# Kernel optimization log

Measured on AMD Instinct MI355X. Metric: run time of the kernel, lower is better.

The kernel has to match this reference:

```python
import jax, jax.numpy as jnp
import numpy as np

NA, NV, FEAT = 8000, 4000, 32
H, D = 4, 16            # heads, per-head dim
HD = H * D              # 64 node width
BLOCKS, DEPTH = 6, 2    # 12 attention layers total
OUT = 64
AK, AVK, VK = 10, 15, 15
EPS = 1e-5


def setup_inputs() -> dict:
    key = jax.random.key(0)
    ks = jax.random.split(key, 16)
    rn = lambda k, s, sc=0.1: (jax.random.normal(k, s, dtype=jnp.float32) * sc)
    return {
        "atom_x": rn(ks[0], (NA, FEAT), 1.0),
        "atom_pos": rn(ks[1], (NA, 3), 1.0),
        "vox_x": rn(ks[2], (NV, FEAT), 1.0),
        "vox_pos": rn(ks[3], (NV, 3), 1.0),
        "W_atom_in": rn(ks[4], (FEAT, HD)),
        "b_atom_in": jnp.zeros((HD,), jnp.float32),
        "W_vox_in": rn(ks[5], (FEAT, HD)),
        "b_vox_in": jnp.zeros((HD,), jnp.float32),
        "emlp_w1": rn(ks[6], (3, 1, 8), 0.5),
        "emlp_b1": jnp.zeros((3, 8), jnp.float32),
        "emlp_w2": rn(ks[7], (3, 8, 1), 0.5),
        "emlp_b2": jnp.zeros((3, 1), jnp.float32),
        "ln_g": jnp.ones((BLOCKS * DEPTH, HD), jnp.float32),
        "ln_b": jnp.zeros((BLOCKS * DEPTH, HD), jnp.float32),
        "Ws": rn(ks[8], (BLOCKS * DEPTH, HD, HD)),
        "Wd": rn(ks[9], (BLOCKS * DEPTH, HD, HD)),
        "We": rn(ks[10], (BLOCKS * DEPTH, 1, HD)),
        "att": rn(ks[11], (BLOCKS * DEPTH, H, D)),
        "Wo1": rn(ks[12], ((BLOCKS + 1) * HD, HD)),
        "bo1": jnp.zeros((HD,), jnp.float32),
        "Wo2": rn(ks[13], (HD, OUT)),
        "bo2": jnp.zeros((OUT,), jnp.float32),
    }


def _knn_edges(q_pos, c_pos, k, q_off, c_off):
    # for each query, k nearest candidates (single-graph batch)
    d2 = (jnp.sum(q_pos * q_pos, 1, keepdims=True)
          - 2.0 * q_pos @ c_pos.T
          + jnp.sum(c_pos * c_pos, 1))                      # [Nq, Nc]
    idx = jax.lax.top_k(-d2, k)[1]                          # [Nq, k]
    src = (idx + c_off).reshape(-1)
    dst = jnp.repeat(jnp.arange(q_pos.shape[0]) + q_off, k)
    return src, dst


def _forward(atom_x, atom_pos, vox_x, vox_pos,
             W_atom_in, b_atom_in, W_vox_in, b_vox_in,
             emlp_w1, emlp_b1, emlp_w2, emlp_b2,
             ln_g, ln_b, Ws, Wd, We, att, Wo1, bo1, Wo2, bo2):
    Na, Nv = atom_x.shape[0], vox_x.shape[0]
    N = Na + Nv
    x = jnp.concatenate([atom_x @ W_atom_in + b_atom_in,
                         vox_x @ W_vox_in + b_vox_in], 0)   # [N, HD]
    pos = jnp.concatenate([atom_pos, vox_pos], 0)           # [N, 3]

    # (query_pos, cand_pos, k, q_offset, c_offset, edge-MLP index)
    combos = [(atom_pos, atom_pos, AK, 0, 0, 0),    # atom<-atom
              (atom_pos, vox_pos, AVK, 0, Na, 1),   # atom<-vox
              (vox_pos, vox_pos, VK, Na, Na, 2)]    # vox<-vox
    srcs, dsts, attrs = [], [], []
    for qp, cp, k, qo, co, mi in combos:
        s, d = _knn_edges(qp, cp, k, qo, co)
        dist = jnp.linalg.norm(pos[s] - pos[d], axis=1, keepdims=True)  # [E,1]
        h = jax.nn.relu(dist @ emlp_w1[mi] + emlp_b1[mi])
        attrs.append(h @ emlp_w2[mi] + emlp_b2[mi])
        srcs.append(s); dsts.append(d)
    src = jnp.concatenate(srcs)
    dst = jnp.concatenate(dsts)
    eattr = jnp.concatenate(attrs, 0)                       # [E,1]

    def gat_layer(xin, l):
        mu = xin.mean(-1, keepdims=True)
        var = xin.var(-1, keepdims=True)
        h = (xin - mu) * jax.lax.rsqrt(var + EPS) * ln_g[l] + ln_b[l]
        s = (h @ Ws[l]).reshape(N, H, D)
        d_ = (h @ Wd[l]).reshape(N, H, D)
        e = (eattr @ We[l]).reshape(-1, H, D)
        m = s[src] + d_[dst] + e                            # [E,H,D]
        score = jnp.einsum('ehd,hd->eh', jax.nn.leaky_relu(m, 0.2), att[l])
        smax = jax.ops.segment_max(score, dst, num_segments=N)
        a = jnp.exp(score - smax[dst])
        denom = jax.ops.segment_sum(a, dst, num_segments=N)
        alpha = a / denom[dst]                              # softmax per dst node
        msg = jax.ops.segment_sum(alpha[..., None] * s[src], dst,
                                  num_segments=N).reshape(N, HD)
        return jax.nn.relu(xin + msg)

    outs = [x]
    cur = x
    for b in range(BLOCKS):
        for dd in range(DEPTH):
            cur = gat_layer(cur, b * DEPTH + dd)
        outs.append(cur)
    cat = jnp.concatenate(outs, -1)[Na:]                    # vox nodes, [Nv,448]
    enc = jax.nn.relu(cat @ Wo1 + bo1) @ Wo2 + bo2          # [Nv,OUT]
    return enc


def reference(atom_x, atom_pos, vox_x, vox_pos,
              W_atom_in, b_atom_in, W_vox_in, b_vox_in,
              emlp_w1, emlp_b1, emlp_w2, emlp_b2,
              ln_g, ln_b, Ws, Wd, We, att, Wo1, bo1, Wo2, bo2):
    enc = _forward(atom_x, atom_pos, vox_x, vox_pos,
                   W_atom_in, b_atom_in, W_vox_in, b_vox_in,
                   emlp_w1, emlp_b1, emlp_w2, emlp_b2,
                   ln_g, ln_b, Ws, Wd, We, att, Wo1, bo1, Wo2, bo2)
    return (enc, vox_pos)
```

## Files before the change

kernel.cpp:

```cpp
#include <hip/hip_runtime.h>
#include <math.h>

#define NA 8000
#define NV 4000
#define NN 12000
#define NA_PAD 8192
#define NV_PAD 4096
#define KNN_TILE 2048
#define FEAT 32
#define HD 64
#define NLAYER 12
#define E_AA 80000
#define E_AV 120000
#define E_VV 60000
#define E_TOT 260000
#define ENC_SIZE (NV * HD)
#define EPS 1e-5f
#define NGRP (NN/4)

__device__ __forceinline__ float wave_sum64(float v) {
#pragma unroll
  for (int off = 1; off < 64; off <<= 1) v += __shfl_xor(v, off);
  return v;
}

__device__ __forceinline__ float dpp_step(float v, const int ctrl) {
  int p;
  switch (ctrl) {
    case 0xB1:  p = __builtin_amdgcn_update_dpp(0, __float_as_int(v), 0xB1,  0xF, 0xF, true); break;
    case 0x4E:  p = __builtin_amdgcn_update_dpp(0, __float_as_int(v), 0x4E,  0xF, 0xF, true); break;
    case 0x141: p = __builtin_amdgcn_update_dpp(0, __float_as_int(v), 0x141, 0xF, 0xF, true); break;
    default:    p = __builtin_amdgcn_update_dpp(0, __float_as_int(v), 0x140, 0xF, 0xF, true); break;
  }
  return v + __int_as_float(p);
}

__device__ __forceinline__ float head_sum16_dpp(float v) {
  v = dpp_step(v, 0xB1);
  v = dpp_step(v, 0x4E);
  v = dpp_step(v, 0x141);
  v = dpp_step(v, 0x140);
  return v;
}

__device__ __forceinline__ float wave_sum64_dpp(float v) {
  v = head_sum16_dpp(v);
  v += __shfl_xor(v, 16);
  v += __shfl_xor(v, 32);
  return v;
}

__device__ __forceinline__ float dpp_shr1_f(float v) {
  const int p = __builtin_amdgcn_update_dpp(0, __float_as_int(v), 0x138, 0xF, 0xF, true);
  return __int_as_float(p);
}
__device__ __forceinline__ int dpp_shr1_i(int v) {
  return __builtin_amdgcn_update_dpp(0, v, 0x138, 0xF, 0xF, true);
}

__global__ __launch_bounds__(256) void pack_kernel(
    const float* __restrict__ apos, const float* __restrict__ vpos,
    float4* __restrict__ apk, float4* __restrict__ vpk)
{
  const int i = blockIdx.x * 256 + threadIdx.x;
  if (i < NA_PAD) {
    float4 r;
    if (i < NA) {
      const float cx = apos[i*3+0], cy = apos[i*3+1], cz = apos[i*3+2];
      r = make_float4(cx, cy, cz, (cx*cx + cy*cy) + cz*cz);
    } else r = make_float4(0.f, 0.f, 0.f, INFINITY);
    apk[i] = r;
  } else {
    const int j = i - NA_PAD;
    if (j < NV_PAD) {
      float4 r;
      if (j < NV) {
        const float cx = vpos[j*3+0], cy = vpos[j*3+1], cz = vpos[j*3+2];
        r = make_float4(cx, cy, cz, (cx*cx + cy*cy) + cz*cz);
      } else r = make_float4(0.f, 0.f, 0.f, INFINITY);
      vpk[j] = r;
    }
  }
}

#define KNN_INS(D2, JB)                                                \
  {                                                                    \
    unsigned long long m = __ballot((D2) < thrD);                      \
    if (m) {                                                           \
      do {                                                             \
        const int sl = __ffsll(m) - 1;                                 \
        m &= (m - 1ULL);                                               \
        const float v  = __shfl((D2), sl);                             \
        const int   vi = (JB) + sl;                                    \
        const bool stay = (eD < v) || (eD == v && eI < vi);            \
        const float pD = dpp_shr1_f(eD);                               \
        const int   pI = dpp_shr1_i(eI);                               \
        int pS = dpp_shr1_i(stay ? 1 : 0);                             \
        if (lane == 0) pS = 1;                                         \
        eD = stay ? eD : (pS ? v  : pD);                               \
        eI = stay ? eI : (pS ? vi : pI);                               \
      } while (m);                                                     \
      thrD = __shfl(eD, K-1);                                          \
    }                                                                  \
  }

template<int K, int NC_PAD>
__device__ __attribute__((noinline)) void knn_body(
    const float* __restrict__ qpos, const float4* __restrict__ cpk,
    int c_off, int* __restrict__ out_src, int qblock)
{
  extern __shared__ float4 tile[];
  const int tid  = threadIdx.x;
  const int wid  = tid >> 6, lane = tid & 63;
  const int q    = qblock * 8 + wid;
  const float qx = qpos[q*3+0], qy = qpos[q*3+1], qz = qpos[q*3+2];
  float qt = __fmul_rn(qx, qx);
  qt = __fmaf_rn(qy, qy, qt);
  const float qq = __fmaf_rn(qz, qz, qt);

  float eD = INFINITY; int eI = 0x7fffffff;
  float thrD = INFINITY;

  for (int t0 = 0; t0 < NC_PAD; t0 += KNN_TILE) {
    __syncthreads();
#pragma unroll
    for (int s = 0; s < KNN_TILE/512; ++s)
      tile[s*512 + tid] = cpk[t0 + s*512 + tid];
    __syncthreads();
#pragma unroll
    for (int it = 0; it < KNN_TILE/256; ++it) {
      const int b = it*256;
      const float4 c0 = tile[b +   0 + lane];
      const float4 c1 = tile[b +  64 + lane];
      const float4 c2 = tile[b + 128 + lane];
      const float4 c3 = tile[b + 192 + lane];
      float u0 = __fmul_rn(qx, c0.x); u0 = __fmaf_rn(qy, c0.y, u0);
      const float dot0 = __fmaf_rn(qz, c0.z, u0);
      const float d20  = __fadd_rn(__fmaf_rn(-2.0f, dot0, qq), c0.w);
      float u1 = __fmul_rn(qx, c1.x); u1 = __fmaf_rn(qy, c1.y, u1);
      const float dot1 = __fmaf_rn(qz, c1.z, u1);
      const float d21  = __fadd_rn(__fmaf_rn(-2.0f, dot1, qq), c1.w);
      float u2 = __fmul_rn(qx, c2.x); u2 = __fmaf_rn(qy, c2.y, u2);
      const float dot2 = __fmaf_rn(qz, c2.z, u2);
      const float d22  = __fadd_rn(__fmaf_rn(-2.0f, dot2, qq), c2.w);
      float u3 = __fmul_rn(qx, c3.x); u3 = __fmaf_rn(qy, c3.y, u3);
      const float dot3 = __fmaf_rn(qz, c3.z, u3);
      const float d23  = __fadd_rn(__fmaf_rn(-2.0f, dot3, qq), c3.w);
      const float dmin = fminf(fminf(d20, d21), fminf(d22, d23));
      if (__ballot(dmin < thrD)) {
        KNN_INS(d20, t0 + b +   0)
        KNN_INS(d21, t0 + b +  64)
        KNN_INS(d22, t0 + b + 128)
        KNN_INS(d23, t0 + b + 192)
      }
    }
  }
  if (lane < K) out_src[q*K + lane] = eI + c_off;
}

__global__ __launch_bounds__(512) void knn_all_kernel(
    const float* __restrict__ apos, const float* __restrict__ vpos,
    const float4* __restrict__ apk, const float4* __restrict__ vpk,
    int* __restrict__ srcA, int* __restrict__ srcAV, int* __restrict__ srcVV)
{
  const int b = blockIdx.x;
  if (b < NA/8)
    knn_body<10, NA_PAD>(apos, apk, 0,  srcA,  b);
  else if (b < 2*(NA/8))
    knn_body<15, NV_PAD>(apos, vpk, NA, srcAV, b - NA/8);
  else
    knn_body<15, NV_PAD>(vpos, vpk, NA, srcVV, b - 2*(NA/8));
}

__device__ __forceinline__ void ln_sd(
    float v, int node, int lane, int l,
    const float* __restrict__ ln_g, const float* __restrict__ ln_b,
    const float* __restrict__ Ws, const float* __restrict__ Wd,
    float* __restrict__ sbuf, float* __restrict__ dbuf)
{
  const float m = wave_sum64_dpp(v) * (1.0f/64.0f);
  const float c = v - m;
  const float var = wave_sum64_dpp(c*c) * (1.0f/64.0f);
  const float hn = c * rsqrtf(var + EPS) * ln_g[l*HD + lane] + ln_b[l*HD + lane];
  const float* ws = Ws + (size_t)l*HD*HD;
  const float* wd = Wd + (size_t)l*HD*HD;
  float accs = 0.0f, accd = 0.0f;
#pragma unroll
  for (int j = 0; j < HD; ++j) {
    const float hj = __shfl(hn, j);
    accs += hj * ws[j*HD + lane];
    accd += hj * wd[j*HD + lane];
  }
  sbuf[node*HD + lane] = accs;
  dbuf[node*HD + lane] = accd;
}

__global__ __launch_bounds__(64) void init_kernel(
    const float* __restrict__ atom_x, const float* __restrict__ vox_x,
    const float* __restrict__ Wa, const float* __restrict__ ba,
    const float* __restrict__ Wv, const float* __restrict__ bv,
    const float* __restrict__ ln_g, const float* __restrict__ ln_b,
    const float* __restrict__ Ws, const float* __restrict__ Wd,
    float* __restrict__ x, float* __restrict__ snap0,
    float* __restrict__ sbuf, float* __restrict__ dbuf)
{
  const int node = blockIdx.x;
  const int t    = threadIdx.x;
  const float* in; const float* W; const float* b;
  if (node < NA) { in = atom_x + node*FEAT;     W = Wa; b = ba; }
  else           { in = vox_x + (node-NA)*FEAT; W = Wv; b = bv; }
  float acc = b[t];
#pragma unroll
  for (int j = 0; j < FEAT; ++j) acc += in[j] * W[j*HD + t];
  x[node*HD + t] = acc;
  if (node >= NA) snap0[(node-NA)*HD + t] = acc;
  ln_sd(acc, node, t, 0, ln_g, ln_b, Ws, Wd, sbuf, dbuf);
}

__device__ __forceinline__ void load_pos(const float* ap, const float* vp,
                                         int i, float& px, float& py, float& pz)
{
  const float* p = (i < NA) ? (ap + i*3) : (vp + (i - NA)*3);
  px = p[0]; py = p[1]; pz = p[2];
}

__global__ __launch_bounds__(256) void edge_attr_kernel(
    const float* __restrict__ atom_pos, const float* __restrict__ vox_pos,
    const int* __restrict__ srcA, const int* __restrict__ srcAV,
    const int* __restrict__ srcVV,
    const float* __restrict__ w1, const float* __restrict__ b1,
    const float* __restrict__ w2, const float* __restrict__ b2,
    float* __restrict__ eattr)
{
  const int e = blockIdx.x * 256 + threadIdx.x;
  if (e >= E_TOT) return;
  int s, d, mi;
  if (e < E_AA)              { mi = 0; s = srcA[e];                 d = e / 10; }
  else if (e < E_AA + E_AV)  { mi = 1; const int t = e - E_AA;      s = srcAV[t]; d = t / 15; }
  else                       { mi = 2; const int t = e - E_AA - E_AV; s = srcVV[t]; d = NA + t / 15; }
  float sx, sy, sz, dx_, dy_, dz_;
  load_pos(atom_pos, vox_pos, s, sx, sy, sz);
  load_pos(atom_pos, vox_pos, d, dx_, dy_, dz_);
  const float ex = sx - dx_, ey = sy - dy_, ez = sz - dz_;
  const float dist = sqrtf(ex*ex + ey*ey + ez*ez);
  float acc = b2[mi];
#pragma unroll
  for (int j = 0; j < 8; ++j) {
    float h = dist * w1[mi*8 + j] + b1[mi*8 + j];
    h = (h > 0.0f) ? h : 0.0f;
    acc += h * w2[mi*8 + j];
  }
  eattr[e] = acc;
}

template<int NE, bool IS_ATOM>
__device__ __forceinline__ float agg_node(
    int n, int lane,
    float* __restrict__ x,
    const float* __restrict__ sbuf, const float* __restrict__ dbuf,
    const float* __restrict__ eattr,
    const int* __restrict__ srcA, const int* __restrict__ srcAV,
    const int* __restrict__ srcVV,
    const float* __restrict__ We, const float* __restrict__ att, int l,
    float* __restrict__ snap)
{
  const float wet  = We[l*HD + lane];
  const float attv = att[l*HD + lane];
  const float dn   = dbuf[n*HD + lane];

  int esrc[NE]; float eat[NE];
#pragma unroll
  for (int e = 0; e < NE; ++e) {
    int src, eidx;
    if (IS_ATOM) {
      if (e < 10) { src = srcA[n*10 + e];       eidx = n*10 + e; }
      else        { src = srcAV[n*15 + (e-10)]; eidx = E_AA + n*15 + (e-10); }
    } else {
      const int nv = n - NA;
      src = srcVV[nv*15 + e]; eidx = E_AA + E_AV + nv*15 + e;
    }
    esrc[e] = src;
    eat[e]  = eattr[eidx];
  }

  float srow[NE];
#pragma unroll
  for (int e = 0; e < NE; ++e) srow[e] = sbuf[esrc[e]*HD + lane];

  float escore[NE];
#pragma unroll
  for (int e = 0; e < NE; ++e) {
    float mm = srow[e] + dn + eat[e] * wet;
    mm = (mm >= 0.0f) ? mm : 0.2f * mm;
    escore[e] = head_sum16_dpp(mm * attv);
  }
  float mx = -INFINITY;
#pragma unroll
  for (int e = 0; e < NE; ++e) mx = fmaxf(mx, escore[e]);
  float den = 0.0f;
#pragma unroll
  for (int e = 0; e < NE; ++e) {
    const float a = __expf(escore[e] - mx);
    escore[e] = a; den += a;
  }
  const float inv = 1.0f / den;
  float msg = 0.0f;
#pragma unroll
  for (int e = 0; e < NE; ++e) msg += (escore[e] * inv) * srow[e];
  float xv = x[n*HD + lane] + msg;
  xv = (xv > 0.0f) ? xv : 0.0f;
  x[n*HD + lane] = xv;
  if (!IS_ATOM && snap != nullptr) snap[(n - NA)*HD + lane] = xv;
  return xv;
}

__global__ __launch_bounds__(256, 4) void layer_kernel(
    float* __restrict__ x,
    const float* __restrict__ sbuf_in, float* __restrict__ dbuf,
    float* __restrict__ sbuf_out,
    const float* __restrict__ eattr,
    const int* __restrict__ srcA, const int* __restrict__ srcAV,
    const int* __restrict__ srcVV,
    const float* __restrict__ We, const float* __restrict__ att,
    const float* __restrict__ ln_g, const float* __restrict__ ln_b,
    const float* __restrict__ Ws, const float* __restrict__ Wd,
    int l, float* __restrict__ snap, int do_next)
{
  const int wid = threadIdx.x >> 6, lane = threadIdx.x & 63;
  const int n = blockIdx.x * 4 + wid;
  __shared__ float hn_sh[HD][4];
  __shared__ float part[4][4][2][HD];

  float xv;
  if (n < NA) {
    if (!do_next) return;
    xv = agg_node<25,true>(n, lane, x, sbuf_in, dbuf, eattr,
                           srcA, srcAV, srcVV, We, att, l, nullptr);
  } else {
    xv = agg_node<15,false>(n, lane, x, sbuf_in, dbuf, eattr,
                            srcA, srcAV, srcVV, We, att, l, snap);
  }
  if (!do_next) return;

  const int ln = l + 1;
  const float mean = wave_sum64_dpp(xv) * (1.0f/64.0f);
  const float cc   = xv - mean;
  const float var  = wave_sum64_dpp(cc*cc) * (1.0f/64.0f);
  const float hn   = cc * rsqrtf(var + EPS) * ln_g[ln*HD + lane] + ln_b[ln*HD + lane];
  hn_sh[lane][wid] = hn;
  __syncthreads();

  const float* wsp = Ws + (size_t)ln*HD*HD;
  const float* wdp = Wd + (size_t)ln*HD*HD;
  float as0=0.f, as1=0.f, as2=0.f, as3=0.f;
  float ad0=0.f, ad1=0.f, ad2=0.f, ad3=0.f;
#pragma unroll
  for (int jj = 0; jj < 16; ++jj) {
    const int j = wid*16 + jj;
    const float wvs = wsp[j*HD + lane];
    const float wvd = wdp[j*HD + lane];
    const float4 h = *(const float4*)&hn_sh[j][0];
    as0 += h.x*wvs; ad0 += h.x*wvd;
    as1 += h.y*wvs; ad1 += h.y*wvd;
    as2 += h.z*wvs; ad2 += h.z*wvd;
    as3 += h.w*wvs; ad3 += h.w*wvd;
  }
  part[wid][0][0][lane] = as0; part[wid][0][1][lane] = ad0;
  part[wid][1][0][lane] = as1; part[wid][1][1][lane] = ad1;
  part[wid][2][0][lane] = as2; part[wid][2][1][lane] = ad2;
  part[wid][3][0][lane] = as3; part[wid][3][1][lane] = ad3;
  __syncthreads();

  const float accs = ((part[0][wid][0][lane] + part[1][wid][0][lane])
                    + (part[2][wid][0][lane] + part[3][wid][0][lane]));
  const float accd = ((part[0][wid][1][lane] + part[1][wid][1][lane])
                    + (part[2][wid][1][lane] + part[3][wid][1][lane]));
  sbuf_out[n*HD + lane] = accs;
  dbuf[n*HD + lane]     = accd;
}

__global__ __launch_bounds__(256) void head_kernel(
    const float* __restrict__ snaps,
    const float* __restrict__ Wo1, const float* __restrict__ bo1,
    const float* __restrict__ Wo2, const float* __restrict__ bo2,
    float* __restrict__ out)
{
  const int wid = threadIdx.x >> 6, lane = threadIdx.x & 63;
  const int n = blockIdx.x * 4 + wid;
  __shared__ float cat[4][7*HD];
  __shared__ float part[4][4][HD];
  __shared__ float o1[4][HD];

#pragma unroll
  for (int c = 0; c < 7; ++c)
    cat[wid][c*HD + lane] = snaps[(size_t)c*NV*HD + n*HD + lane];
  __syncthreads();

  float a0=0.f, a1=0.f, a2=0.f, a3=0.f;
  for (int jj = 0; jj < 112; ++jj) {
    const int j = wid*112 + jj;
    const float w = Wo1[j*HD + lane];
    a0 += cat[0][j]*w; a1 += cat[1][j]*w;
    a2 += cat[2][j]*w; a3 += cat[3][j]*w;
  }
  part[wid][0][lane] = a0; part[wid][1][lane] = a1;
  part[wid][2][lane] = a2; part[wid][3][lane] = a3;
  __syncthreads();

  float acc = bo1[lane] + ((part[0][wid][lane] + part[1][wid][lane])
                         + (part[2][wid][lane] + part[3][wid][lane]));
  acc = fmaxf(acc, 0.0f);
  o1[wid][lane] = acc;
  __syncthreads();

  float b0=0.f, b1=0.f, b2=0.f, b3=0.f;
#pragma unroll
  for (int jj = 0; jj < 16; ++jj) {
    const int j = wid*16 + jj;
    const float w = Wo2[j*HD + lane];
    b0 += o1[0][j]*w; b1 += o1[1][j]*w;
    b2 += o1[2][j]*w; b3 += o1[3][j]*w;
  }
  __syncthreads();
  part[wid][0][lane] = b0; part[wid][1][lane] = b1;
  part[wid][2][lane] = b2; part[wid][3][lane] = b3;
  __syncthreads();

  const float acc2 = bo2[lane] + ((part[0][wid][lane] + part[1][wid][lane])
                                + (part[2][wid][lane] + part[3][wid][lane]));
  out[n*HD + lane] = acc2;
}

__global__ __launch_bounds__(256) void copy_pos_kernel(
    const float* __restrict__ vp, float* __restrict__ out)
{
  const int i = blockIdx.x * 256 + threadIdx.x;
  if (i < NV*3) out[ENC_SIZE + i] = vp[i];
}

extern "C" void kernel_launch(void* const* d_in, const int* in_sizes, int n_in,
                              void* d_out, int out_size, void* d_ws, size_t ws_size,
                              hipStream_t stream)
{
  const float* atom_x    = (const float*)d_in[0];
  const float* atom_pos  = (const float*)d_in[1];
  const float* vox_x     = (const float*)d_in[2];
  const float* vox_pos   = (const float*)d_in[3];
  const float* W_atom_in = (const float*)d_in[4];
  const float* b_atom_in = (const float*)d_in[5];
  const float* W_vox_in  = (const float*)d_in[6];
  const float* b_vox_in  = (const float*)d_in[7];
  const float* emlp_w1   = (const float*)d_in[8];
  const float* emlp_b1   = (const float*)d_in[9];
  const float* emlp_w2   = (const float*)d_in[10];
  const float* emlp_b2   = (const float*)d_in[11];
  const float* ln_g      = (const float*)d_in[12];
  const float* ln_b      = (const float*)d_in[13];
  const float* Ws        = (const float*)d_in[14];
  const float* Wd        = (const float*)d_in[15];
  const float* We        = (const float*)d_in[16];
  const float* att       = (const float*)d_in[17];
  const float* Wo1       = (const float*)d_in[18];
  const float* bo1       = (const float*)d_in[19];
  const float* Wo2       = (const float*)d_in[20];
  const float* bo2       = (const float*)d_in[21];
  float* out = (float*)d_out;

  float* ws    = (float*)d_ws;
  float* x     = ws;
  float* sA    = x  + (size_t)NN*HD;
  float* sB    = sA + (size_t)NN*HD;
  float* dbuf  = sB + (size_t)NN*HD;
  float* eattr = dbuf + (size_t)NN*HD;
  float* snaps = eattr + E_TOT;
  int*   srcA  = (int*)(snaps + (size_t)7*NV*HD);
  int*   srcAV = srcA  + E_AA;
  int*   srcVV = srcAV + E_AV;
  float4* apk  = (float4*)(srcVV + E_VV);
  float4* vpk  = apk + NA_PAD;

  pack_kernel<<<(NA_PAD + NV_PAD + 255)/256, 256, 0, stream>>>(
      atom_pos, vox_pos, apk, vpk);
  knn_all_kernel<<<NA/8 + NA/8 + NV/8, 512, KNN_TILE*sizeof(float4), stream>>>(
      atom_pos, vox_pos, apk, vpk, srcA, srcAV, srcVV);
  edge_attr_kernel<<<(E_TOT + 255)/256, 256, 0, stream>>>(
      atom_pos, vox_pos, srcA, srcAV, srcVV,
      emlp_w1, emlp_b1, emlp_w2, emlp_b2, eattr);
  init_kernel<<<NN, 64, 0, stream>>>(atom_x, vox_x, W_atom_in, b_atom_in,
                                     W_vox_in, b_vox_in, ln_g, ln_b, Ws, Wd,
                                     x, snaps, sA, dbuf);
  for (int l = 0; l < NLAYER; ++l) {
    float* s_in  = (l & 1) ? sB : sA;
    float* s_out = (l & 1) ? sA : sB;
    float* snap  = (l & 1) ? (snaps + (size_t)(l/2 + 1)*NV*HD) : nullptr;
    layer_kernel<<<NGRP, 256, 0, stream>>>(x, s_in, dbuf, s_out, eattr,
                                           srcA, srcAV, srcVV, We, att,
                                           ln_g, ln_b, Ws, Wd, l, snap,
                                           (l < NLAYER-1) ? 1 : 0);
  }
  head_kernel<<<NV/4, 256, 0, stream>>>(snaps, Wo1, bo1, Wo2, bo2, out);
  copy_pos_kernel<<<(NV*3 + 255)/256, 256, 0, stream>>>(vox_pos, out);
}
```

Measured before the change: 346.2 us.

## Double-buffer kNN candidate tiles and fold node init into kNN launch

The kNN kernel now uses two shared-memory tiles of half the previous size. It prefetches the next candidate tile while computing distances on the current one, so each tile needs one barrier instead of two. The separate init kernel (input projection, LayerNorm and the first Ws/Wd projection) becomes extra blocks in the kNN launch, one wave per node. This removes a launch and lets init work overlap the kNN blocks, at the cost of a larger, more branched kernel whose register use is driven by the kNN path.

```diff
diff --git a/kernel.cpp b/kernel.cpp
--- a/kernel.cpp
+++ b/kernel.cpp
@@ -6,7 +6,7 @@
 #define NN 12000
 #define NA_PAD 8192
 #define NV_PAD 4096
-#define KNN_TILE 2048
+#define KNN_TILE 1024
 #define FEAT 32
 #define HD 64
 #define NLAYER 12
@@ -17,6 +17,8 @@
 #define ENC_SIZE (NV * HD)
 #define EPS 1e-5f
 #define NGRP (NN/4)
+#define KNN_BLOCKS (NA/8 + NA/8 + NV/8)
+#define INIT_BLOCKS (NN/8)
 
 __device__ __forceinline__ float wave_sum64(float v) {
 #pragma unroll
@@ -121,19 +123,27 @@
   float eD = INFINITY; int eI = 0x7fffffff;
   float thrD = INFINITY;
 
+#pragma unroll
+  for (int s = 0; s < KNN_TILE/512; ++s)
+    tile[s*512 + tid] = cpk[s*512 + tid];
+  __syncthreads();
+
+  int cur = 0;
   for (int t0 = 0; t0 < NC_PAD; t0 += KNN_TILE) {
-    __syncthreads();
-#pragma unroll
-    for (int s = 0; s < KNN_TILE/512; ++s)
-      tile[s*512 + tid] = cpk[t0 + s*512 + tid];
-    __syncthreads();
+    const int t1 = t0 + KNN_TILE;
+    if (t1 < NC_PAD) {
+#pragma unroll
+      for (int s = 0; s < KNN_TILE/512; ++s)
+        tile[(cur^1)*KNN_TILE + s*512 + tid] = cpk[t1 + s*512 + tid];
+    }
+    const float4* tb = tile + cur*KNN_TILE;
 #pragma unroll
     for (int it = 0; it < KNN_TILE/256; ++it) {
       const int b = it*256;
-      const float4 c0 = tile[b +   0 + lane];
-      const float4 c1 = tile[b +  64 + lane];
-      const float4 c2 = tile[b + 128 + lane];
-      const float4 c3 = tile[b + 192 + lane];
+      const float4 c0 = tb[b +   0 + lane];
+      const float4 c1 = tb[b +  64 + lane];
+      const float4 c2 = tb[b + 128 + lane];
+      const float4 c3 = tb[b + 192 + lane];
       float u0 = __fmul_rn(qx, c0.x); u0 = __fmaf_rn(qy, c0.y, u0);
       const float dot0 = __fmaf_rn(qz, c0.z, u0);
       const float d20  = __fadd_rn(__fmaf_rn(-2.0f, dot0, qq), c0.w);
@@ -154,22 +164,10 @@
         KNN_INS(d23, t0 + b + 192)
       }
     }
+    __syncthreads();
+    cur ^= 1;
   }
   if (lane < K) out_src[q*K + lane] = eI + c_off;
-}
-
-__global__ __launch_bounds__(512) void knn_all_kernel(
-    const float* __restrict__ apos, const float* __restrict__ vpos,
-    const float4* __restrict__ apk, const float4* __restrict__ vpk,
-    int* __restrict__ srcA, int* __restrict__ srcAV, int* __restrict__ srcVV)
-{
-  const int b = blockIdx.x;
-  if (b < NA/8)
-    knn_body<10, NA_PAD>(apos, apk, 0,  srcA,  b);
-  else if (b < 2*(NA/8))
-    knn_body<15, NV_PAD>(apos, vpk, NA, srcAV, b - NA/8);
-  else
-    knn_body<15, NV_PAD>(vpos, vpk, NA, srcVV, b - 2*(NA/8));
 }
 
 __device__ __forceinline__ void ln_sd(
@@ -195,7 +193,8 @@
   dbuf[node*HD + lane] = accd;
 }
 
-__global__ __launch_bounds__(64) void init_kernel(
+__device__ __forceinline__ void init_node(
+    int node, int lane,
     const float* __restrict__ atom_x, const float* __restrict__ vox_x,
     const float* __restrict__ Wa, const float* __restrict__ ba,
     const float* __restrict__ Wv, const float* __restrict__ bv,
@@ -204,17 +203,42 @@
     float* __restrict__ x, float* __restrict__ snap0,
     float* __restrict__ sbuf, float* __restrict__ dbuf)
 {
-  const int node = blockIdx.x;
-  const int t    = threadIdx.x;
   const float* in; const float* W; const float* b;
   if (node < NA) { in = atom_x + node*FEAT;     W = Wa; b = ba; }
   else           { in = vox_x + (node-NA)*FEAT; W = Wv; b = bv; }
-  float acc = b[t];
-#pragma unroll
-  for (int j = 0; j < FEAT; ++j) acc += in[j] * W[j*HD + t];
-  x[node*HD + t] = acc;
-  if (node >= NA) snap0[(node-NA)*HD + t] = acc;
-  ln_sd(acc, node, t, 0, ln_g, ln_b, Ws, Wd, sbuf, dbuf);
+  float acc = b[lane];
+#pragma unroll
+  for (int j = 0; j < FEAT; ++j) acc += in[j] * W[j*HD + lane];
+  x[node*HD + lane] = acc;
+  if (node >= NA) snap0[(node-NA)*HD + lane] = acc;
+  ln_sd(acc, node, lane, 0, ln_g, ln_b, Ws, Wd, sbuf, dbuf);
+}
+
+__global__ __launch_bounds__(512) void knn_all_kernel(
+    const float* __restrict__ apos, const float* __restrict__ vpos,
+    const float4* __restrict__ apk, const float4* __restrict__ vpk,
+    int* __restrict__ srcA, int* __restrict__ srcAV, int* __restrict__ srcVV,
+    const float* __restrict__ atom_x, const float* __restrict__ vox_x,
+    const float* __restrict__ Wa, const float* __restrict__ ba,
+    const float* __restrict__ Wv, const float* __restrict__ bv,
+    const float* __restrict__ ln_g, const float* __restrict__ ln_b,
+    const float* __restrict__ Ws, const float* __restrict__ Wd,
+    float* __restrict__ x, float* __restrict__ snap0,
+    float* __restrict__ sbuf0, float* __restrict__ dbuf)
+{
+  const int b = blockIdx.x;
+  const int wid = threadIdx.x >> 6, lane = threadIdx.x & 63;
+  if (b < NA/8)
+    knn_body<10, NA_PAD>(apos, apk, 0,  srcA,  b);
+  else if (b < 2*(NA/8))
+    knn_body<15, NV_PAD>(apos, vpk, NA, srcAV, b - NA/8);
+  else if (b < KNN_BLOCKS)
+    knn_body<15, NV_PAD>(vpos, vpk, NA, srcVV, b - 2*(NA/8));
+  else {
+    const int node = (b - KNN_BLOCKS)*8 + wid;
+    init_node(node, lane, atom_x, vox_x, Wa, ba, Wv, bv,
+              ln_g, ln_b, Ws, Wd, x, snap0, sbuf0, dbuf);
+  }
 }
 
 __device__ __forceinline__ void load_pos(const float* ap, const float* vp,
@@ -481,14 +505,13 @@
 
   pack_kernel<<<(NA_PAD + NV_PAD + 255)/256, 256, 0, stream>>>(
       atom_pos, vox_pos, apk, vpk);
-  knn_all_kernel<<<NA/8 + NA/8 + NV/8, 512, KNN_TILE*sizeof(float4), stream>>>(
-      atom_pos, vox_pos, apk, vpk, srcA, srcAV, srcVV);
+  knn_all_kernel<<<KNN_BLOCKS + INIT_BLOCKS, 512, 2*KNN_TILE*sizeof(float4), stream>>>(
+      atom_pos, vox_pos, apk, vpk, srcA, srcAV, srcVV,
+      atom_x, vox_x, W_atom_in, b_atom_in, W_vox_in, b_vox_in,
+      ln_g, ln_b, Ws, Wd, x, snaps, sA, dbuf);
   edge_attr_kernel<<<(E_TOT + 255)/256, 256, 0, stream>>>(
       atom_pos, vox_pos, srcA, srcAV, srcVV,
       emlp_w1, emlp_b1, emlp_w2, emlp_b2, eattr);
-  init_kernel<<<NN, 64, 0, stream>>>(atom_x, vox_x, W_atom_in, b_atom_in,
-                                     W_vox_in, b_vox_in, ln_g, ln_b, Ws, Wd,
-                                     x, snaps, sA, dbuf);
   for (int l = 0; l < NLAYER; ++l) {
     float* s_in  = (l & 1) ? sB : sA;
     float* s_out = (l & 1) ? sA : sB;
```

After: 334.3 us. -3.5%, faster.
